# Performance work log

Measured on AMD Instinct MI355X. Metric: run time of the kernel, lower is better.

The kernel has to match this reference:

```python
import jax, jax.numpy as jnp
import numpy as np

D_MODEL = 1024
NUM_HEADS = 16
HEAD_DIM = D_MODEL // NUM_HEADS
ALPHA = 1.0


def setup_inputs() -> dict:
    key = jax.random.key(0)
    ks = jax.random.split(key, 9)
    B, T, D = 2, 2048, D_MODEL
    s = 1.0 / np.sqrt(D)
    inp = {
        "x": jax.random.normal(ks[0], (B, T, D), dtype=jnp.float32),
        "Wq": jax.random.uniform(ks[1], (D, D), jnp.float32, -s, s),
        "bq": jax.random.uniform(ks[2], (D,), jnp.float32, -s, s),
        "Wk": jax.random.uniform(ks[3], (D, D), jnp.float32, -s, s),
        "bk": jax.random.uniform(ks[4], (D,), jnp.float32, -s, s),
        "Wv": jax.random.uniform(ks[5], (D, D), jnp.float32, -s, s),
        "bv": jax.random.uniform(ks[6], (D,), jnp.float32, -s, s),
        "Wo": jax.random.uniform(ks[7], (D, D), jnp.float32, -s, s),
        "bo": jax.random.uniform(ks[8], (D,), jnp.float32, -s, s),
    }
    return inp


def reference(x, Wq, bq, Wk, bk, Wv, bv, Wo, bo):
    B, T, D = x.shape
    H, hd = NUM_HEADS, HEAD_DIM

    def split_heads(y):  # [B,T,D] -> [B,H,T,hd]
        return y.reshape(B, T, H, hd).transpose(0, 2, 1, 3)

    Q = split_heads(x @ Wq.T + bq)
    K = split_heads(x @ Wk.T + bk)
    V = split_heads(x @ Wv.T + bv)

    scores = jnp.einsum('bhid,bhjd->bhij', Q, K) / jnp.sqrt(jnp.float32(hd))

    t = jnp.arange(T)
    delta = t[:, None] - t[None, :]  # [T,T], i - j
    causal_mask = delta < 0          # j > i (strict upper triangle)
    # similarity_power_law decay bias: -(delta)^alpha for delta >= 0, else 0
    decay = jnp.where(causal_mask, 0.0, -(delta.astype(jnp.float32) ** ALPHA))

    scores = jnp.where(causal_mask, -jnp.inf, scores) + decay
    attn = jax.nn.softmax(scores, axis=-1)

    out = jnp.einsum('bhij,bhjd->bhid', attn, V)
    out = out.transpose(0, 2, 1, 3).reshape(B, T, D)
    return out @ Wo.T + bo
```

## Files before the change

### kernel.cpp

```cpp
#include <hip/hip_runtime.h>

#define TT 2048
#define DD 1024
#define HH 16
#define HD 64
#define NTOK 4096

typedef __bf16 bf16x8 __attribute__((ext_vector_type(8)));
typedef short short4v __attribute__((ext_vector_type(4)));
typedef float f32x4 __attribute__((ext_vector_type(4)));
typedef unsigned short ushort8v __attribute__((ext_vector_type(8)));

__device__ __forceinline__ unsigned short f2bf(float f) {
  unsigned u = __float_as_uint(f);
  u += 0x7fffu + ((u >> 16) & 1u);
  return (unsigned short)(u >> 16);
}

#if __has_builtin(__builtin_amdgcn_mfma_f32_16x16x16bf16_1k)
__device__ __forceinline__ f32x4 mfma16(short4v a, short4v b, f32x4 c) {
  return __builtin_amdgcn_mfma_f32_16x16x16bf16_1k(a, b, c, 0, 0, 0);
}
#else
__device__ __forceinline__ f32x4 mfma16(short4v a, short4v b, f32x4 c) {
  asm("v_mfma_f32_16x16x16_bf16 %0, %1, %2, %0\n\ts_nop 7\n\ts_nop 7"
      : "+v"(c) : "v"(a), "v"(b));
  return c;
}
#endif

typedef void __attribute__((address_space(1))) as1_void;
typedef void __attribute__((address_space(3))) as3_void;
__device__ __forceinline__ void gl_lds16(const void* g, void* l) {
  __builtin_amdgcn_global_load_lds((as1_void*)g, (as3_void*)l, 16, 0, 0);
}

__global__ __launch_bounds__(256)
void wcmha_cast_all(const float4* __restrict__ x,  const float4* __restrict__ wq,
                    const float4* __restrict__ wk, const float4* __restrict__ wv,
                    const float4* __restrict__ wo,
                    ushort8v* __restrict__ xb,  ushort8v* __restrict__ wqb,
                    ushort8v* __restrict__ wkb, ushort8v* __restrict__ wvb,
                    ushort8v* __restrict__ wob) {
  const int i = blockIdx.x * 256 + threadIdx.x;
  const float4* src;
  ushort8v* dst;
  int off;
  if (i < 524288) {
    src = x; dst = xb; off = i;
  } else {
    int j = i - 524288;
    int sel = j >> 17;
    off = j & 131071;
    const float4* ws_[4] = {wq, wk, wv, wo};
    ushort8v* wd_[4] = {wqb, wkb, wvb, wob};
    src = ws_[sel]; dst = wd_[sel];
  }
  float4 a = src[off * 2];
  float4 b = src[off * 2 + 1];
  ushort8v o;
  o[0] = f2bf(a.x); o[1] = f2bf(a.y); o[2] = f2bf(a.z); o[3] = f2bf(a.w);
  o[4] = f2bf(b.x); o[5] = f2bf(b.y); o[6] = f2bf(b.z); o[7] = f2bf(b.w);
  dst[off] = o;
}

template <int BN_, bool SWAP>
__device__ __forceinline__ void gemm_db(const unsigned short* __restrict__ X,
                                        const unsigned short* __restrict__ W,
                                        int m0, int n0,
                                        unsigned short* As, unsigned short* Bs,
                                        f32x4 acc[4][BN_ / 32]) {
  constexpr int NI = BN_ / 32;
  constexpr int JB = (BN_ * 4) / 256;
  const int tid = threadIdx.x, wid = tid >> 6, lane = tid & 63;
  const int m = lane & 15, quad = lane >> 4;
  const int wm = (wid >> 1) * 64, wn = (wid & 1) * (BN_ / 2);
  const int xq = (quad ^ ((m >> 1) & 3)) * 8;

  const unsigned short* gA[2];
  const unsigned short* gB[JB];
#pragma unroll
  for (int j = 0; j < 2; ++j) {
    int c = wid * 64 + lane + j * 256;
    gA[j] = X + (size_t)(m0 + (c >> 2)) * DD + ((c & 3) ^ ((c >> 3) & 3)) * 8;
  }
#pragma unroll
  for (int j = 0; j < JB; ++j) {
    int c = wid * 64 + lane + j * 256;
    gB[j] = W + (size_t)(n0 + (c >> 2)) * DD + ((c & 3) ^ ((c >> 3) & 3)) * 8;
  }
  unsigned short* lA[2][2];
  unsigned short* lB[2][JB];
#pragma unroll
  for (int p = 0; p < 2; ++p) {
#pragma unroll
    for (int j = 0; j < 2; ++j)
      lA[p][j] = As + p * (128 * 32) + (wid * 64 + j * 256) * 8;
#pragma unroll
    for (int j = 0; j < JB; ++j)
      lB[p][j] = Bs + p * (BN_ * 32) + (wid * 64 + j * 256) * 8;
  }

#pragma unroll
  for (int i = 0; i < 4; ++i)
#pragma unroll
    for (int j = 0; j < NI; ++j) acc[i][j] = (f32x4){0.f, 0.f, 0.f, 0.f};

#pragma unroll
  for (int j = 0; j < 2; ++j) gl_lds16(gA[j], lA[0][j]);
#pragma unroll
  for (int j = 0; j < JB; ++j) gl_lds16(gB[j], lB[0][j]);

  for (int k = 0; k < 32; ++k) {
    const int p = k & 1;
    __syncthreads();
    if (k < 31) {
      const int k1 = (k + 1) * 32;
#pragma unroll
      for (int j = 0; j < 2; ++j) gl_lds16(gA[j] + k1, lA[p ^ 1][j]);
#pragma unroll
      for (int j = 0; j < JB; ++j) gl_lds16(gB[j] + k1, lB[p ^ 1][j]);
    }
    const unsigned short* ap = As + p * (128 * 32);
    const unsigned short* bp = Bs + p * (BN_ * 32);
    bf16x8 af[4], bf[NI];
#pragma unroll
    for (int mi = 0; mi < 4; ++mi)
      af[mi] = *(const bf16x8*)&ap[(wm + mi * 16 + m) * 32 + xq];
#pragma unroll
    for (int ni = 0; ni < NI; ++ni)
      bf[ni] = *(const bf16x8*)&bp[(wn + ni * 16 + m) * 32 + xq];
#pragma unroll
    for (int mi = 0; mi < 4; ++mi)
#pragma unroll
      for (int ni = 0; ni < NI; ++ni)
        acc[mi][ni] = SWAP
            ? __builtin_amdgcn_mfma_f32_16x16x32_bf16(bf[ni], af[mi], acc[mi][ni], 0, 0, 0)
            : __builtin_amdgcn_mfma_f32_16x16x32_bf16(af[mi], bf[ni], acc[mi][ni], 0, 0, 0);
  }
}

__global__ __launch_bounds__(256)
void wcmha_gemm_qkv(const unsigned short* __restrict__ X,
                    const unsigned short* __restrict__ Wq,
                    const unsigned short* __restrict__ Wk,
                    const unsigned short* __restrict__ Wv,
                    const float* __restrict__ bq, const float* __restrict__ bk,
                    const float* __restrict__ bv,
                    unsigned short* __restrict__ Qb,
                    unsigned short* __restrict__ Kb,
                    unsigned short* __restrict__ Vt) {
  __shared__ unsigned short As[2 * 128 * 32];
  __shared__ unsigned short Bs[2 * 128 * 32];
  const int mat = blockIdx.y >> 3;
  const int m0 = blockIdx.x * 128;
  const int n0 = (blockIdx.y & 7) * 128;

  const int lane = threadIdx.x & 63, wid = threadIdx.x >> 6;
  const int m = lane & 15, quad = lane >> 4;
  const int wm = (wid >> 1) * 64, wn = (wid & 1) * 64;

  f32x4 acc[4][4];
  if (mat < 2) {
    const unsigned short* W = mat ? Wk : Wq;
    const float* bias = mat ? bk : bq;
    unsigned short* dst = mat ? Kb : Qb;
    gemm_db<128, true>(X, W, m0, n0, As, Bs, acc);
#pragma unroll
    for (int mi = 0; mi < 4; ++mi) {
      int row = m0 + wm + mi * 16 + m;
      int b = row >> 11, t = row & (TT - 1);
#pragma unroll
      for (int ni = 0; ni < 4; ++ni) {
        int col0 = n0 + wn + ni * 16 + quad * 4;
        int h = col0 >> 6, d0 = col0 & 63;
        float4 bb = *(const float4*)&bias[col0];
        short4v v;
        v[0] = (short)f2bf(acc[mi][ni][0] + bb.x);
        v[1] = (short)f2bf(acc[mi][ni][1] + bb.y);
        v[2] = (short)f2bf(acc[mi][ni][2] + bb.z);
        v[3] = (short)f2bf(acc[mi][ni][3] + bb.w);
        *(short4v*)&dst[((size_t)(b * HH + h) * TT + t) * HD + d0] = v;
      }
    }
  } else {
    gemm_db<128, false>(X, Wv, m0, n0, As, Bs, acc);
#pragma unroll
    for (int ni = 0; ni < 4; ++ni) {
      int col = n0 + wn + ni * 16 + m;
      int h = col >> 6, d = col & 63;
      float bb = bv[col];
#pragma unroll
      for (int mi = 0; mi < 4; ++mi) {
        int row0 = m0 + wm + mi * 16 + quad * 4;
        int b = row0 >> 11, t0 = row0 & (TT - 1);
        short4v v;
#pragma unroll
        for (int r = 0; r < 4; ++r) v[r] = (short)f2bf(acc[mi][ni][r] + bb);
        *(short4v*)&Vt[((size_t)(b * HH + h) * HD + d) * TT + t0] = v;
      }
    }
  }
}

__global__ __launch_bounds__(256)
void wcmha_gemm_out(const unsigned short* __restrict__ X,
                    const unsigned short* __restrict__ W,
                    const float* __restrict__ bias,
                    float* __restrict__ Y) {
  __shared__ unsigned short As[2 * 128 * 32];
  __shared__ unsigned short Bs[2 * 128 * 32];
  const int m0 = blockIdx.x * 128;
  const int n0 = blockIdx.y * 128;
  const int lane = threadIdx.x & 63, wid = threadIdx.x >> 6;
  const int m = lane & 15, quad = lane >> 4;
  const int wm = (wid >> 1) * 64, wn = (wid & 1) * 64;

  f32x4 acc[4][4];
  gemm_db<128, true>(X, W, m0, n0, As, Bs, acc);

#pragma unroll
  for (int mi = 0; mi < 4; ++mi) {
    int row = m0 + wm + mi * 16 + m;
#pragma unroll
    for (int ni = 0; ni < 4; ++ni) {
      int col0 = n0 + wn + ni * 16 + quad * 4;
      float4 bb = *(const float4*)&bias[col0];
      float4 o;
      o.x = acc[mi][ni][0] + bb.x;
      o.y = acc[mi][ni][1] + bb.y;
      o.z = acc[mi][ni][2] + bb.z;
      o.w = acc[mi][ni][3] + bb.w;
      *(float4*)&Y[(size_t)row * DD + col0] = o;
    }
  }
}

__global__ __launch_bounds__(256)
void wcmha_attn(const unsigned short* __restrict__ Qb,
                const unsigned short* __restrict__ Kb,
                const unsigned short* __restrict__ Vt,
                unsigned short* __restrict__ O) {
  const int wid = threadIdx.x >> 6, lane = threadIdx.x & 63;
  const int gw = (blockIdx.x << 2) + wid;
  const int qt = gw & 127, bh = gw >> 7;
  const int qbase = qt << 4;
  const int il = lane & 15, quad = lane >> 4;
  const int ig = qbase + il;

  const unsigned short* q_ptr = Qb + (size_t)bh * TT * HD;
  const unsigned short* k_ptr = Kb + (size_t)bh * TT * HD;
  const unsigned short* v_ptr = Vt + (size_t)bh * HD * TT;

  const bf16x8 qf0 = *(const bf16x8*)(q_ptr + (size_t)ig * HD + quad * 8);
  const bf16x8 qf1 = *(const bf16x8*)(q_ptr + (size_t)ig * HD + 32 + quad * 8);

  const int j0 = (qbase >= 48) ? qbase - 48 : 0;

  f32x4 st[4];
#pragma unroll
  for (int jt = 0; jt < 4; ++jt) {
    const unsigned short* kp = k_ptr + (size_t)(j0 + jt * 16 + il) * HD;
    bf16x8 k0 = *(const bf16x8*)(kp + quad * 8);
    bf16x8 k1 = *(const bf16x8*)(kp + 32 + quad * 8);
    f32x4 a = {0.f, 0.f, 0.f, 0.f};
    a = __builtin_amdgcn_mfma_f32_16x16x32_bf16(k0, qf0, a, 0, 0, 0);
    a = __builtin_amdgcn_mfma_f32_16x16x32_bf16(k1, qf1, a, 0, 0, 0);
    st[jt] = a;
  }

  float mloc = -3.0e38f;
#pragma unroll
  for (int jt = 0; jt < 4; ++jt)
#pragma unroll
    for (int r = 0; r < 4; ++r) {
      int jg = j0 + jt * 16 + quad * 4 + r;
      float v = (jg > ig) ? -3.0e38f : st[jt][r] * 0.125f - (float)(ig - jg);
      st[jt][r] = v;
      mloc = fmaxf(mloc, v);
    }
  mloc = fmaxf(mloc, __shfl_xor(mloc, 16));
  mloc = fmaxf(mloc, __shfl_xor(mloc, 32));

  float rs = 0.f;
  short4v pf[4];
#pragma unroll
  for (int jt = 0; jt < 4; ++jt)
#pragma unroll
    for (int r = 0; r < 4; ++r) {
      float p = __expf(st[jt][r] - mloc);
      rs += p;
      pf[jt][r] = (short)f2bf(p);
    }
  rs += __shfl_xor(rs, 16);
  rs += __shfl_xor(rs, 32);

  f32x4 o_acc[4];
#pragma unroll
  for (int nt = 0; nt < 4; ++nt) o_acc[nt] = (f32x4){0.f, 0.f, 0.f, 0.f};
#pragma unroll
  for (int jt = 0; jt < 4; ++jt)
#pragma unroll
    for (int nt = 0; nt < 4; ++nt) {
      short4v vf = *(const short4v*)(v_ptr + (size_t)(nt * 16 + il) * TT +
                                     j0 + jt * 16 + quad * 4);
      o_acc[nt] = mfma16(vf, pf[jt], o_acc[nt]);
    }

  const float inv_l = 1.f / rs;
  const int b = bh >> 4, hh = bh & 15;
  unsigned short* ob = O + ((size_t)(b * TT + ig)) * DD + hh * HD;
#pragma unroll
  for (int nt = 0; nt < 4; ++nt) {
    short4v v;
#pragma unroll
    for (int r = 0; r < 4; ++r) v[r] = (short)f2bf(o_acc[nt][r] * inv_l);
    *(short4v*)&ob[nt * 16 + quad * 4] = v;
  }
}

extern "C" void kernel_launch(void* const* d_in, const int* in_sizes, int n_in,
                              void* d_out, int out_size, void* d_ws, size_t ws_size,
                              hipStream_t stream) {
  const float* x  = (const float*)d_in[0];
  const float* Wq = (const float*)d_in[1];
  const float* bq = (const float*)d_in[2];
  const float* Wk = (const float*)d_in[3];
  const float* bk = (const float*)d_in[4];
  const float* Wv = (const float*)d_in[5];
  const float* bv = (const float*)d_in[6];
  const float* Wo = (const float*)d_in[7];
  const float* bo = (const float*)d_in[8];

  char* ws = (char*)d_ws;
  unsigned short* xb  = (unsigned short*)(ws);
  unsigned short* wqb = (unsigned short*)(ws + (8u << 20));
  unsigned short* wkb = wqb + (1u << 20);
  unsigned short* wvb = wkb + (1u << 20);
  unsigned short* wob = wvb + (1u << 20);
  unsigned short* Qb  = (unsigned short*)(ws + (16u << 20));
  unsigned short* Kb  = (unsigned short*)(ws + (24u << 20));
  unsigned short* Vt  = (unsigned short*)(ws + (32u << 20));
  unsigned short* Ob  = xb;

  wcmha_cast_all<<<4096, 256, 0, stream>>>(
      (const float4*)x, (const float4*)Wq, (const float4*)Wk,
      (const float4*)Wv, (const float4*)Wo,
      (ushort8v*)xb, (ushort8v*)wqb, (ushort8v*)wkb, (ushort8v*)wvb,
      (ushort8v*)wob);

  wcmha_gemm_qkv<<<dim3(32, 24), 256, 0, stream>>>(xb, wqb, wkb, wvb,
                                                   bq, bk, bv, Qb, Kb, Vt);

  wcmha_attn<<<1024, 256, 0, stream>>>(Qb, Kb, Vt, Ob);

  wcmha_gemm_out<<<dim3(32, 8), 256, 0, stream>>>(Ob, wob, bo, (float*)d_out);
}
```

Before: 167.2 us.

## Fuse cast, QKV GEMM, attention and output GEMM into one persistent kernel

Replaces the four separate launches with a single persistent kernel of 768 blocks. The stages are separated by a software grid barrier built on an atomic counter, and each stage uses grid-stride or block-index remapping. The goal is to remove per-launch overhead and the drain/fill gaps between kernels. The output GEMM is also retiled to 128x64 tiles over 512 blocks. The change relies on all 768 blocks being co-resident (launch bounds of 3 blocks per CU); if they are not, the barrier deadlocks. The occupancy hint may also constrain registers in the GEMM and attention phases.

```diff
diff --git a/kernel.cpp b/kernel.cpp
--- a/kernel.cpp
+++ b/kernel.cpp
@@ -5,6 +5,7 @@
 #define HH 16
 #define HD 64
 #define NTOK 4096
+#define NBLK 768
 
 typedef __bf16 bf16x8 __attribute__((ext_vector_type(8)));
 typedef short short4v __attribute__((ext_vector_type(4)));
@@ -35,33 +36,21 @@
   __builtin_amdgcn_global_load_lds((as1_void*)g, (as3_void*)l, 16, 0, 0);
 }
 
-__global__ __launch_bounds__(256)
-void wcmha_cast_all(const float4* __restrict__ x,  const float4* __restrict__ wq,
-                    const float4* __restrict__ wk, const float4* __restrict__ wv,
-                    const float4* __restrict__ wo,
-                    ushort8v* __restrict__ xb,  ushort8v* __restrict__ wqb,
-                    ushort8v* __restrict__ wkb, ushort8v* __restrict__ wvb,
-                    ushort8v* __restrict__ wob) {
-  const int i = blockIdx.x * 256 + threadIdx.x;
-  const float4* src;
-  ushort8v* dst;
-  int off;
-  if (i < 524288) {
-    src = x; dst = xb; off = i;
-  } else {
-    int j = i - 524288;
-    int sel = j >> 17;
-    off = j & 131071;
-    const float4* ws_[4] = {wq, wk, wv, wo};
-    ushort8v* wd_[4] = {wqb, wkb, wvb, wob};
-    src = ws_[sel]; dst = wd_[sel];
-  }
-  float4 a = src[off * 2];
-  float4 b = src[off * 2 + 1];
-  ushort8v o;
-  o[0] = f2bf(a.x); o[1] = f2bf(a.y); o[2] = f2bf(a.z); o[3] = f2bf(a.w);
-  o[4] = f2bf(b.x); o[5] = f2bf(b.y); o[6] = f2bf(b.z); o[7] = f2bf(b.w);
-  dst[off] = o;
+__device__ unsigned g_bar = 0;
+
+__device__ __forceinline__ void grid_sync() {
+  __syncthreads();
+  if (threadIdx.x == 0) {
+    __builtin_amdgcn_fence(__ATOMIC_RELEASE, "agent");
+    unsigned old = __hip_atomic_fetch_add(&g_bar, 1u, __ATOMIC_RELAXED,
+                                          __HIP_MEMORY_SCOPE_AGENT);
+    unsigned target = (old / NBLK + 1u) * NBLK;
+    while (__hip_atomic_load(&g_bar, __ATOMIC_RELAXED,
+                             __HIP_MEMORY_SCOPE_AGENT) < target)
+      __builtin_amdgcn_s_sleep(1);
+    __builtin_amdgcn_fence(__ATOMIC_ACQUIRE, "agent");
+  }
+  __syncthreads();
 }
 
 template <int BN_, bool SWAP>
@@ -140,182 +129,208 @@
   }
 }
 
-__global__ __launch_bounds__(256)
-void wcmha_gemm_qkv(const unsigned short* __restrict__ X,
-                    const unsigned short* __restrict__ Wq,
-                    const unsigned short* __restrict__ Wk,
-                    const unsigned short* __restrict__ Wv,
-                    const float* __restrict__ bq, const float* __restrict__ bk,
-                    const float* __restrict__ bv,
-                    unsigned short* __restrict__ Qb,
-                    unsigned short* __restrict__ Kb,
-                    unsigned short* __restrict__ Vt) {
+__global__ __launch_bounds__(256, 3)
+void wcmha_fused(const float4* __restrict__ xf,  const float4* __restrict__ wqf,
+                 const float4* __restrict__ wkf, const float4* __restrict__ wvf,
+                 const float4* __restrict__ wof,
+                 const float* __restrict__ bq, const float* __restrict__ bk,
+                 const float* __restrict__ bv, const float* __restrict__ bo,
+                 unsigned short* __restrict__ xb,  unsigned short* __restrict__ wqb,
+                 unsigned short* __restrict__ wkb, unsigned short* __restrict__ wvb,
+                 unsigned short* __restrict__ wob,
+                 unsigned short* __restrict__ Qb, unsigned short* __restrict__ Kb,
+                 unsigned short* __restrict__ Vt, float* __restrict__ Y) {
   __shared__ unsigned short As[2 * 128 * 32];
   __shared__ unsigned short Bs[2 * 128 * 32];
-  const int mat = blockIdx.y >> 3;
-  const int m0 = blockIdx.x * 128;
-  const int n0 = (blockIdx.y & 7) * 128;
-
-  const int lane = threadIdx.x & 63, wid = threadIdx.x >> 6;
+
+  const int tid = threadIdx.x;
+  const int lane = tid & 63, wid = tid >> 6;
   const int m = lane & 15, quad = lane >> 4;
-  const int wm = (wid >> 1) * 64, wn = (wid & 1) * 64;
-
-  f32x4 acc[4][4];
-  if (mat < 2) {
-    const unsigned short* W = mat ? Wk : Wq;
-    const float* bias = mat ? bk : bq;
-    unsigned short* dst = mat ? Kb : Qb;
-    gemm_db<128, true>(X, W, m0, n0, As, Bs, acc);
+
+  for (int i = (int)blockIdx.x * 256 + tid; i < 1048576; i += NBLK * 256) {
+    const float4* src;
+    ushort8v* dst;
+    int off;
+    if (i < 524288) {
+      src = xf; dst = (ushort8v*)xb; off = i;
+    } else {
+      int j = i - 524288;
+      int sel = j >> 17;
+      off = j & 131071;
+      const float4* ws_[4] = {wqf, wkf, wvf, wof};
+      ushort8v* wd_[4] = {(ushort8v*)wqb, (ushort8v*)wkb, (ushort8v*)wvb,
+                          (ushort8v*)wob};
+      src = ws_[sel]; dst = wd_[sel];
+    }
+    float4 a = src[off * 2];
+    float4 b = src[off * 2 + 1];
+    ushort8v o;
+    o[0] = f2bf(a.x); o[1] = f2bf(a.y); o[2] = f2bf(a.z); o[3] = f2bf(a.w);
+    o[4] = f2bf(b.x); o[5] = f2bf(b.y); o[6] = f2bf(b.z); o[7] = f2bf(b.w);
+    dst[off] = o;
+  }
+
+  grid_sync();
+
+  {
+    const int bx = (int)blockIdx.x & 31;
+    const int by = (int)blockIdx.x >> 5;
+    const int mat = by >> 3;
+    const int m0 = bx * 128;
+    const int n0 = (by & 7) * 128;
+    const int wm = (wid >> 1) * 64, wn = (wid & 1) * 64;
+
+    f32x4 acc[4][4];
+    if (mat < 2) {
+      const unsigned short* W = mat ? wkb : wqb;
+      const float* bias = mat ? bk : bq;
+      unsigned short* dst = mat ? Kb : Qb;
+      gemm_db<128, true>(xb, W, m0, n0, As, Bs, acc);
+#pragma unroll
+      for (int mi = 0; mi < 4; ++mi) {
+        int row = m0 + wm + mi * 16 + m;
+        int b = row >> 11, t = row & (TT - 1);
+#pragma unroll
+        for (int ni = 0; ni < 4; ++ni) {
+          int col0 = n0 + wn + ni * 16 + quad * 4;
+          int h = col0 >> 6, d0 = col0 & 63;
+          float4 bb = *(const float4*)&bias[col0];
+          short4v v;
+          v[0] = (short)f2bf(acc[mi][ni][0] + bb.x);
+          v[1] = (short)f2bf(acc[mi][ni][1] + bb.y);
+          v[2] = (short)f2bf(acc[mi][ni][2] + bb.z);
+          v[3] = (short)f2bf(acc[mi][ni][3] + bb.w);
+          *(short4v*)&dst[((size_t)(b * HH + h) * TT + t) * HD + d0] = v;
+        }
+      }
+    } else {
+      gemm_db<128, false>(xb, wvb, m0, n0, As, Bs, acc);
+#pragma unroll
+      for (int ni = 0; ni < 4; ++ni) {
+        int col = n0 + wn + ni * 16 + m;
+        int h = col >> 6, d = col & 63;
+        float bb = bv[col];
+#pragma unroll
+        for (int mi = 0; mi < 4; ++mi) {
+          int row0 = m0 + wm + mi * 16 + quad * 4;
+          int b = row0 >> 11, t0 = row0 & (TT - 1);
+          short4v v;
+#pragma unroll
+          for (int r = 0; r < 4; ++r) v[r] = (short)f2bf(acc[mi][ni][r] + bb);
+          *(short4v*)&Vt[((size_t)(b * HH + h) * HD + d) * TT + t0] = v;
+        }
+      }
+    }
+  }
+
+  grid_sync();
+
+  {
+    unsigned short* O = xb;
+    const int il = m;
+    for (int gw = ((int)blockIdx.x << 2) + wid; gw < 4096; gw += NBLK * 4) {
+      const int qt = gw & 127, bh = gw >> 7;
+      const int qbase = qt << 4;
+      const int ig = qbase + il;
+
+      const unsigned short* q_ptr = Qb + (size_t)bh * TT * HD;
+      const unsigned short* k_ptr = Kb + (size_t)bh * TT * HD;
+      const unsigned short* v_ptr = Vt + (size_t)bh * HD * TT;
+
+      const bf16x8 qf0 = *(const bf16x8*)(q_ptr + (size_t)ig * HD + quad * 8);
+      const bf16x8 qf1 = *(const bf16x8*)(q_ptr + (size_t)ig * HD + 32 + quad * 8);
+
+      const int j0 = (qbase >= 48) ? qbase - 48 : 0;
+
+      f32x4 st[4];
+#pragma unroll
+      for (int jt = 0; jt < 4; ++jt) {
+        const unsigned short* kp = k_ptr + (size_t)(j0 + jt * 16 + il) * HD;
+        bf16x8 k0 = *(const bf16x8*)(kp + quad * 8);
+        bf16x8 k1 = *(const bf16x8*)(kp + 32 + quad * 8);
+        f32x4 a = {0.f, 0.f, 0.f, 0.f};
+        a = __builtin_amdgcn_mfma_f32_16x16x32_bf16(k0, qf0, a, 0, 0, 0);
+        a = __builtin_amdgcn_mfma_f32_16x16x32_bf16(k1, qf1, a, 0, 0, 0);
+        st[jt] = a;
+      }
+
+      float mloc = -3.0e38f;
+#pragma unroll
+      for (int jt = 0; jt < 4; ++jt)
+#pragma unroll
+        for (int r = 0; r < 4; ++r) {
+          int jg = j0 + jt * 16 + quad * 4 + r;
+          float v = (jg > ig) ? -3.0e38f : st[jt][r] * 0.125f - (float)(ig - jg);
+          st[jt][r] = v;
+          mloc = fmaxf(mloc, v);
+        }
+      mloc = fmaxf(mloc, __shfl_xor(mloc, 16));
+      mloc = fmaxf(mloc, __shfl_xor(mloc, 32));
+
+      float rs = 0.f;
+      short4v pf[4];
+#pragma unroll
+      for (int jt = 0; jt < 4; ++jt)
+#pragma unroll
+        for (int r = 0; r < 4; ++r) {
+          float p = __expf(st[jt][r] - mloc);
+          rs += p;
+          pf[jt][r] = (short)f2bf(p);
+        }
+      rs += __shfl_xor(rs, 16);
+      rs += __shfl_xor(rs, 32);
+
+      f32x4 o_acc[4];
+#pragma unroll
+      for (int nt = 0; nt < 4; ++nt) o_acc[nt] = (f32x4){0.f, 0.f, 0.f, 0.f};
+#pragma unroll
+      for (int jt = 0; jt < 4; ++jt)
+#pragma unroll
+        for (int nt = 0; nt < 4; ++nt) {
+          short4v vf = *(const short4v*)(v_ptr + (size_t)(nt * 16 + il) * TT +
+                                         j0 + jt * 16 + quad * 4);
+          o_acc[nt] = mfma16(vf, pf[jt], o_acc[nt]);
+        }
+
+      const float inv_l = 1.f / rs;
+      const int b = bh >> 4, hh = bh & 15;
+      unsigned short* ob = O + ((size_t)(b * TT + ig)) * DD + hh * HD;
+#pragma unroll
+      for (int nt = 0; nt < 4; ++nt) {
+        short4v v;
+#pragma unroll
+        for (int r = 0; r < 4; ++r) v[r] = (short)f2bf(o_acc[nt][r] * inv_l);
+        *(short4v*)&ob[nt * 16 + quad * 4] = v;
+      }
+    }
+  }
+
+  grid_sync();
+
+  if (blockIdx.x < 512) {
+    const unsigned short* Ob = xb;
+    const int m0 = ((int)blockIdx.x & 31) * 128;
+    const int n0 = ((int)blockIdx.x >> 5) * 64;
+    const int wm = (wid >> 1) * 64, wn = (wid & 1) * 32;
+
+    f32x4 acc[4][2];
+    gemm_db<64, true>(Ob, wob, m0, n0, As, Bs, acc);
+
 #pragma unroll
     for (int mi = 0; mi < 4; ++mi) {
       int row = m0 + wm + mi * 16 + m;
-      int b = row >> 11, t = row & (TT - 1);
-#pragma unroll
-      for (int ni = 0; ni < 4; ++ni) {
+#pragma unroll
+      for (int ni = 0; ni < 2; ++ni) {
         int col0 = n0 + wn + ni * 16 + quad * 4;
-        int h = col0 >> 6, d0 = col0 & 63;
-        float4 bb = *(const float4*)&bias[col0];
-        short4v v;
-        v[0] = (short)f2bf(acc[mi][ni][0] + bb.x);
-        v[1] = (short)f2bf(acc[mi][ni][1] + bb.y);
-        v[2] = (short)f2bf(acc[mi][ni][2] + bb.z);
-        v[3] = (short)f2bf(acc[mi][ni][3] + bb.w);
-        *(short4v*)&dst[((size_t)(b * HH + h) * TT + t) * HD + d0] = v;
-      }
-    }
-  } else {
-    gemm_db<128, false>(X, Wv, m0, n0, As, Bs, acc);
-#pragma unroll
-    for (int ni = 0; ni < 4; ++ni) {
-      int col = n0 + wn + ni * 16 + m;
-      int h = col >> 6, d = col & 63;
-      float bb = bv[col];
-#pragma unroll
-      for (int mi = 0; mi < 4; ++mi) {
-        int row0 = m0 + wm + mi * 16 + quad * 4;
-        int b = row0 >> 11, t0 = row0 & (TT - 1);
-        short4v v;
-#pragma unroll
-        for (int r = 0; r < 4; ++r) v[r] = (short)f2bf(acc[mi][ni][r] + bb);
-        *(short4v*)&Vt[((size_t)(b * HH + h) * HD + d) * TT + t0] = v;
-      }
-    }
-  }
-}
-
-__global__ __launch_bounds__(256)
-void wcmha_gemm_out(const unsigned short* __restrict__ X,
-                    const unsigned short* __restrict__ W,
-                    const float* __restrict__ bias,
-                    float* __restrict__ Y) {
-  __shared__ unsigned short As[2 * 128 * 32];
-  __shared__ unsigned short Bs[2 * 128 * 32];
-  const int m0 = blockIdx.x * 128;
-  const int n0 = blockIdx.y * 128;
-  const int lane = threadIdx.x & 63, wid = threadIdx.x >> 6;
-  const int m = lane & 15, quad = lane >> 4;
-  const int wm = (wid >> 1) * 64, wn = (wid & 1) * 64;
-
-  f32x4 acc[4][4];
-  gemm_db<128, true>(X, W, m0, n0, As, Bs, acc);
-
-#pragma unroll
-  for (int mi = 0; mi < 4; ++mi) {
-    int row = m0 + wm + mi * 16 + m;
-#pragma unroll
-    for (int ni = 0; ni < 4; ++ni) {
-      int col0 = n0 + wn + ni * 16 + quad * 4;
-      float4 bb = *(const float4*)&bias[col0];
-      float4 o;
-      o.x = acc[mi][ni][0] + bb.x;
-      o.y = acc[mi][ni][1] + bb.y;
-      o.z = acc[mi][ni][2] + bb.z;
-      o.w = acc[mi][ni][3] + bb.w;
-      *(float4*)&Y[(size_t)row * DD + col0] = o;
-    }
-  }
-}
-
-__global__ __launch_bounds__(256)
-void wcmha_attn(const unsigned short* __restrict__ Qb,
-                const unsigned short* __restrict__ Kb,
-                const unsigned short* __restrict__ Vt,
-                unsigned short* __restrict__ O) {
-  const int wid = threadIdx.x >> 6, lane = threadIdx.x & 63;
-  const int gw = (blockIdx.x << 2) + wid;
-  const int qt = gw & 127, bh = gw >> 7;
-  const int qbase = qt << 4;
-  const int il = lane & 15, quad = lane >> 4;
-  const int ig = qbase + il;
-
-  const unsigned short* q_ptr = Qb + (size_t)bh * TT * HD;
-  const unsigned short* k_ptr = Kb + (size_t)bh * TT * HD;
-  const unsigned short* v_ptr = Vt + (size_t)bh * HD * TT;
-
-  const bf16x8 qf0 = *(const bf16x8*)(q_ptr + (size_t)ig * HD + quad * 8);
-  const bf16x8 qf1 = *(const bf16x8*)(q_ptr + (size_t)ig * HD + 32 + quad * 8);
-
-  const int j0 = (qbase >= 48) ? qbase - 48 : 0;
-
-  f32x4 st[4];
-#pragma unroll
-  for (int jt = 0; jt < 4; ++jt) {
-    const unsigned short* kp = k_ptr + (size_t)(j0 + jt * 16 + il) * HD;
-    bf16x8 k0 = *(const bf16x8*)(kp + quad * 8);
-    bf16x8 k1 = *(const bf16x8*)(kp + 32 + quad * 8);
-    f32x4 a = {0.f, 0.f, 0.f, 0.f};
-    a = __builtin_amdgcn_mfma_f32_16x16x32_bf16(k0, qf0, a, 0, 0, 0);
-    a = __builtin_amdgcn_mfma_f32_16x16x32_bf16(k1, qf1, a, 0, 0, 0);
-    st[jt] = a;
-  }
-
-  float mloc = -3.0e38f;
-#pragma unroll
-  for (int jt = 0; jt < 4; ++jt)
-#pragma unroll
-    for (int r = 0; r < 4; ++r) {
-      int jg = j0 + jt * 16 + quad * 4 + r;
-      float v = (jg > ig) ? -3.0e38f : st[jt][r] * 0.125f - (float)(ig - jg);
-      st[jt][r] = v;
-      mloc = fmaxf(mloc, v);
-    }
-  mloc = fmaxf(mloc, __shfl_xor(mloc, 16));
-  mloc = fmaxf(mloc, __shfl_xor(mloc, 32));
-
-  float rs = 0.f;
-  short4v pf[4];
-#pragma unroll
-  for (int jt = 0; jt < 4; ++jt)
-#pragma unroll
-    for (int r = 0; r < 4; ++r) {
-      float p = __expf(st[jt][r] - mloc);
-      rs += p;
-      pf[jt][r] = (short)f2bf(p);
-    }
-  rs += __shfl_xor(rs, 16);
-  rs += __shfl_xor(rs, 32);
-
-  f32x4 o_acc[4];
-#pragma unroll
-  for (int nt = 0; nt < 4; ++nt) o_acc[nt] = (f32x4){0.f, 0.f, 0.f, 0.f};
-#pragma unroll
-  for (int jt = 0; jt < 4; ++jt)
-#pragma unroll
-    for (int nt = 0; nt < 4; ++nt) {
-      short4v vf = *(const short4v*)(v_ptr + (size_t)(nt * 16 + il) * TT +
-                                     j0 + jt * 16 + quad * 4);
-      o_acc[nt] = mfma16(vf, pf[jt], o_acc[nt]);
-    }
-
-  const float inv_l = 1.f / rs;
-  const int b = bh >> 4, hh = bh & 15;
-  unsigned short* ob = O + ((size_t)(b * TT + ig)) * DD + hh * HD;
-#pragma unroll
-  for (int nt = 0; nt < 4; ++nt) {
-    short4v v;
-#pragma unroll
-    for (int r = 0; r < 4; ++r) v[r] = (short)f2bf(o_acc[nt][r] * inv_l);
-    *(short4v*)&ob[nt * 16 + quad * 4] = v;
+        float4 bb = *(const float4*)&bo[col0];
+        float4 o;
+        o.x = acc[mi][ni][0] + bb.x;
+        o.y = acc[mi][ni][1] + bb.y;
+        o.z = acc[mi][ni][2] + bb.z;
+        o.w = acc[mi][ni][3] + bb.w;
+        *(float4*)&Y[(size_t)row * DD + col0] = o;
+      }
+    }
   }
 }
 
@@ -341,18 +356,10 @@
   unsigned short* Qb  = (unsigned short*)(ws + (16u << 20));
   unsigned short* Kb  = (unsigned short*)(ws + (24u << 20));
   unsigned short* Vt  = (unsigned short*)(ws + (32u << 20));
-  unsigned short* Ob  = xb;
-
-  wcmha_cast_all<<<4096, 256, 0, stream>>>(
+
+  wcmha_fused<<<NBLK, 256, 0, stream>>>(
       (const float4*)x, (const float4*)Wq, (const float4*)Wk,
       (const float4*)Wv, (const float4*)Wo,
-      (ushort8v*)xb, (ushort8v*)wqb, (ushort8v*)wkb, (ushort8v*)wvb,
-      (ushort8v*)wob);
-
-  wcmha_gemm_qkv<<<dim3(32, 24), 256, 0, stream>>>(xb, wqb, wkb, wvb,
-                                                   bq, bk, bv, Qb, Kb, Vt);
-
-  wcmha_attn<<<1024, 256, 0, stream>>>(Qb, Kb, Vt, Ob);
-
-  wcmha_gemm_out<<<dim3(32, 8), 256, 0, stream>>>(Ob, wob, bo, (float*)d_out);
-}
+      bq, bk, bv, bo,
+      xb, wqb, wkb, wvb, wob, Qb, Kb, Vt, (float*)d_out);
+}
```

Measured after the change: 353.1 us. +111.2%, slower.

## Replace QKV GEMM with 256x256 ping-pong pipelined kernel; shrink out-proj tiles

Applied to the files above, without the earlier changes.

The QKV projection now runs as a 512-thread kernel with 256x256 tiles. It uses an explicit four-phase software pipeline: async global-to-LDS loads are interleaved with MFMA bursts, and s_waitcnt, barriers and setprio are placed by hand. This should cut per-tile global traffic and hide load latency better. The V output now uses the same accumulator layout as Q and K, writing the transposed Vt as scalar stores, which may coalesce poorly. The output-projection GEMM switches to 128x64 tiles to launch twice as many blocks, filling more CUs.

```diff
diff --git a/kernel.cpp b/kernel.cpp
--- a/kernel.cpp
+++ b/kernel.cpp
@@ -4,7 +4,6 @@
 #define DD 1024
 #define HH 16
 #define HD 64
-#define NTOK 4096
 
 typedef __bf16 bf16x8 __attribute__((ext_vector_type(8)));
 typedef short short4v __attribute__((ext_vector_type(4)));
@@ -140,39 +139,161 @@
   }
 }
 
-__global__ __launch_bounds__(256)
-void wcmha_gemm_qkv(const unsigned short* __restrict__ X,
-                    const unsigned short* __restrict__ Wq,
-                    const unsigned short* __restrict__ Wk,
-                    const unsigned short* __restrict__ Wv,
-                    const float* __restrict__ bq, const float* __restrict__ bk,
-                    const float* __restrict__ bv,
-                    unsigned short* __restrict__ Qb,
-                    unsigned short* __restrict__ Kb,
-                    unsigned short* __restrict__ Vt) {
-  __shared__ unsigned short As[2 * 128 * 32];
-  __shared__ unsigned short Bs[2 * 128 * 32];
-  const int mat = blockIdx.y >> 3;
-  const int m0 = blockIdx.x * 128;
-  const int n0 = (blockIdx.y & 7) * 128;
-
-  const int lane = threadIdx.x & 63, wid = threadIdx.x >> 6;
+__global__ __launch_bounds__(512, 2)
+void wcmha_qkv8(const unsigned short* __restrict__ X,
+                const unsigned short* __restrict__ Wq,
+                const unsigned short* __restrict__ Wk,
+                const unsigned short* __restrict__ Wv,
+                const float* __restrict__ bq, const float* __restrict__ bk,
+                const float* __restrict__ bv,
+                unsigned short* __restrict__ Qb,
+                unsigned short* __restrict__ Kb,
+                unsigned short* __restrict__ Vt) {
+  __shared__ unsigned short As[2 * 2 * 256 * 32];
+  __shared__ unsigned short Bs[2 * 2 * 256 * 32];
+  const int tid = threadIdx.x;
+  const int lane = tid & 63, wid = tid >> 6;
   const int m = lane & 15, quad = lane >> 4;
-  const int wm = (wid >> 1) * 64, wn = (wid & 1) * 64;
-
-  f32x4 acc[4][4];
+  const int wr = wid >> 2, wc = wid & 3;
+
+  const int mt = blockIdx.x & 15, nt = blockIdx.x >> 4;
+  const int m0 = mt * 256;
+  const int mat = nt >> 2;
+  const int n0w = (nt & 3) * 256;
+  const unsigned short* W = (mat == 0) ? Wq : ((mat == 1) ? Wk : Wv);
+
+  const int srow = tid >> 2;
+  const int schunk = ((tid & 3) ^ ((tid >> 3) & 3)) * 8;
+  const unsigned short* gA[2];
+  const unsigned short* gB[2];
+  gA[0] = X + (size_t)(m0 + srow) * DD + schunk;
+  gA[1] = X + (size_t)(m0 + 128 + srow) * DD + schunk;
+  gB[0] = W + (size_t)(n0w + srow) * DD + schunk;
+  gB[1] = W + (size_t)(n0w + 128 + srow) * DD + schunk;
+  const int ldst = tid * 8;
+
+#define STAGE_A(buf, ks, koff)                                            \
+  {                                                                       \
+    gl_lds16(gA[0] + (koff), &As[((buf) * 2 + (ks)) * 8192 + ldst]);      \
+    gl_lds16(gA[1] + (koff), &As[((buf) * 2 + (ks)) * 8192 + 4096 + ldst]); \
+  }
+#define STAGE_B(buf, ks, koff)                                            \
+  {                                                                       \
+    gl_lds16(gB[0] + (koff), &Bs[((buf) * 2 + (ks)) * 8192 + ldst]);      \
+    gl_lds16(gB[1] + (koff), &Bs[((buf) * 2 + (ks)) * 8192 + 4096 + ldst]); \
+  }
+
+  f32x4 acc[8][4];
+#pragma unroll
+  for (int i = 0; i < 8; ++i)
+#pragma unroll
+    for (int j = 0; j < 4; ++j) acc[i][j] = (f32x4){0.f, 0.f, 0.f, 0.f};
+
+  STAGE_A(0, 0, 0) STAGE_B(0, 0, 0)
+  STAGE_A(0, 1, 32) STAGE_B(0, 1, 32)
+  STAGE_A(1, 0, 64) STAGE_B(1, 0, 64)
+
+  const int xq = (quad ^ ((m >> 1) & 3)) * 8;
+  const int arow = wr * 128 + m;
+  const int brow = wc * 64 + m;
+
+#pragma unroll 1
+  for (int kt = 0; kt < 16; ++kt) {
+    const int cur = kt & 1, nxt = cur ^ 1;
+    const unsigned short* a0 = &As[(cur * 2 + 0) * 8192];
+    const unsigned short* b0 = &Bs[(cur * 2 + 0) * 8192];
+    const unsigned short* a1 = &As[(cur * 2 + 1) * 8192];
+    const unsigned short* b1 = &Bs[(cur * 2 + 1) * 8192];
+    const int kA = (kt + 1) * 64, kB2 = (kt + 2) * 64;
+    bf16x8 af[4], bf[4];
+
+    if (kt < 15) { asm volatile("s_waitcnt vmcnt(8)" ::: "memory"); }
+    else         { asm volatile("s_waitcnt vmcnt(4)" ::: "memory"); }
+    __builtin_amdgcn_s_barrier();
+    __builtin_amdgcn_sched_barrier(0);
+#pragma unroll
+    for (int mi = 0; mi < 4; ++mi)
+      af[mi] = *(const bf16x8*)&a0[(arow + mi * 16) * 32 + xq];
+#pragma unroll
+    for (int ni = 0; ni < 4; ++ni)
+      bf[ni] = *(const bf16x8*)&b0[(brow + ni * 16) * 32 + xq];
+    if (kt < 15) STAGE_A(nxt, 1, kA + 32)
+    asm volatile("s_waitcnt lgkmcnt(0)" ::: "memory");
+    __builtin_amdgcn_sched_barrier(0);
+    __builtin_amdgcn_s_setprio(1);
+#pragma unroll
+    for (int mi = 0; mi < 4; ++mi)
+#pragma unroll
+      for (int ni = 0; ni < 4; ++ni)
+        acc[mi][ni] = __builtin_amdgcn_mfma_f32_16x16x32_bf16(bf[ni], af[mi], acc[mi][ni], 0, 0, 0);
+    __builtin_amdgcn_s_setprio(0);
+
+    __builtin_amdgcn_s_barrier();
+    __builtin_amdgcn_sched_barrier(0);
+#pragma unroll
+    for (int mi = 0; mi < 4; ++mi)
+      af[mi] = *(const bf16x8*)&a0[(arow + (mi + 4) * 16) * 32 + xq];
+    if (kt < 15) STAGE_B(nxt, 1, kA + 32)
+    asm volatile("s_waitcnt lgkmcnt(0)" ::: "memory");
+    __builtin_amdgcn_sched_barrier(0);
+    __builtin_amdgcn_s_setprio(1);
+#pragma unroll
+    for (int mi = 0; mi < 4; ++mi)
+#pragma unroll
+      for (int ni = 0; ni < 4; ++ni)
+        acc[mi + 4][ni] = __builtin_amdgcn_mfma_f32_16x16x32_bf16(bf[ni], af[mi], acc[mi + 4][ni], 0, 0, 0);
+    __builtin_amdgcn_s_setprio(0);
+
+    if (kt < 15) { asm volatile("s_waitcnt vmcnt(8)" ::: "memory"); }
+    else         { asm volatile("s_waitcnt vmcnt(0)" ::: "memory"); }
+    __builtin_amdgcn_s_barrier();
+    __builtin_amdgcn_sched_barrier(0);
+#pragma unroll
+    for (int mi = 0; mi < 4; ++mi)
+      af[mi] = *(const bf16x8*)&a1[(arow + mi * 16) * 32 + xq];
+#pragma unroll
+    for (int ni = 0; ni < 4; ++ni)
+      bf[ni] = *(const bf16x8*)&b1[(brow + ni * 16) * 32 + xq];
+    if (kt < 14) STAGE_A(cur, 0, kB2)
+    asm volatile("s_waitcnt lgkmcnt(0)" ::: "memory");
+    __builtin_amdgcn_sched_barrier(0);
+    __builtin_amdgcn_s_setprio(1);
+#pragma unroll
+    for (int mi = 0; mi < 4; ++mi)
+#pragma unroll
+      for (int ni = 0; ni < 4; ++ni)
+        acc[mi][ni] = __builtin_amdgcn_mfma_f32_16x16x32_bf16(bf[ni], af[mi], acc[mi][ni], 0, 0, 0);
+    __builtin_amdgcn_s_setprio(0);
+
+    __builtin_amdgcn_s_barrier();
+    __builtin_amdgcn_sched_barrier(0);
+#pragma unroll
+    for (int mi = 0; mi < 4; ++mi)
+      af[mi] = *(const bf16x8*)&a1[(arow + (mi + 4) * 16) * 32 + xq];
+    if (kt < 14) STAGE_B(cur, 0, kB2)
+    asm volatile("s_waitcnt lgkmcnt(0)" ::: "memory");
+    __builtin_amdgcn_sched_barrier(0);
+    __builtin_amdgcn_s_setprio(1);
+#pragma unroll
+    for (int mi = 0; mi < 4; ++mi)
+#pragma unroll
+      for (int ni = 0; ni < 4; ++ni)
+        acc[mi + 4][ni] = __builtin_amdgcn_mfma_f32_16x16x32_bf16(bf[ni], af[mi], acc[mi + 4][ni], 0, 0, 0);
+    __builtin_amdgcn_s_setprio(0);
+  }
+#undef STAGE_A
+#undef STAGE_B
+
   if (mat < 2) {
-    const unsigned short* W = mat ? Wk : Wq;
     const float* bias = mat ? bk : bq;
     unsigned short* dst = mat ? Kb : Qb;
-    gemm_db<128, true>(X, W, m0, n0, As, Bs, acc);
-#pragma unroll
-    for (int mi = 0; mi < 4; ++mi) {
-      int row = m0 + wm + mi * 16 + m;
+#pragma unroll
+    for (int mi = 0; mi < 8; ++mi) {
+      int row = m0 + wr * 128 + mi * 16 + m;
       int b = row >> 11, t = row & (TT - 1);
 #pragma unroll
       for (int ni = 0; ni < 4; ++ni) {
-        int col0 = n0 + wn + ni * 16 + quad * 4;
+        int col0 = n0w + wc * 64 + ni * 16 + quad * 4;
         int h = col0 >> 6, d0 = col0 & 63;
         float4 bb = *(const float4*)&bias[col0];
         short4v v;
@@ -184,20 +305,20 @@
       }
     }
   } else {
-    gemm_db<128, false>(X, Wv, m0, n0, As, Bs, acc);
-#pragma unroll
-    for (int ni = 0; ni < 4; ++ni) {
-      int col = n0 + wn + ni * 16 + m;
-      int h = col >> 6, d = col & 63;
-      float bb = bv[col];
-#pragma unroll
-      for (int mi = 0; mi < 4; ++mi) {
-        int row0 = m0 + wm + mi * 16 + quad * 4;
-        int b = row0 >> 11, t0 = row0 & (TT - 1);
-        short4v v;
-#pragma unroll
-        for (int r = 0; r < 4; ++r) v[r] = (short)f2bf(acc[mi][ni][r] + bb);
-        *(short4v*)&Vt[((size_t)(b * HH + h) * HD + d) * TT + t0] = v;
+#pragma unroll
+    for (int mi = 0; mi < 8; ++mi) {
+      int row = m0 + wr * 128 + mi * 16 + m;
+      int b = row >> 11, t = row & (TT - 1);
+#pragma unroll
+      for (int ni = 0; ni < 4; ++ni) {
+        int col0 = n0w + wc * 64 + ni * 16 + quad * 4;
+        int h = col0 >> 6, d0 = col0 & 63;
+#pragma unroll
+        for (int r = 0; r < 4; ++r) {
+          float bb = bv[col0 + r];
+          Vt[((size_t)(b * HH + h) * HD + d0 + r) * TT + t] =
+              f2bf(acc[mi][ni][r] + bb);
+        }
       }
     }
   }
@@ -209,21 +330,21 @@
                     const float* __restrict__ bias,
                     float* __restrict__ Y) {
   __shared__ unsigned short As[2 * 128 * 32];
-  __shared__ unsigned short Bs[2 * 128 * 32];
+  __shared__ unsigned short Bs[2 * 64 * 32];
   const int m0 = blockIdx.x * 128;
-  const int n0 = blockIdx.y * 128;
+  const int n0 = blockIdx.y * 64;
   const int lane = threadIdx.x & 63, wid = threadIdx.x >> 6;
   const int m = lane & 15, quad = lane >> 4;
-  const int wm = (wid >> 1) * 64, wn = (wid & 1) * 64;
-
-  f32x4 acc[4][4];
-  gemm_db<128, true>(X, W, m0, n0, As, Bs, acc);
+  const int wm = (wid >> 1) * 64, wn = (wid & 1) * 32;
+
+  f32x4 acc[4][2];
+  gemm_db<64, true>(X, W, m0, n0, As, Bs, acc);
 
 #pragma unroll
   for (int mi = 0; mi < 4; ++mi) {
     int row = m0 + wm + mi * 16 + m;
 #pragma unroll
-    for (int ni = 0; ni < 4; ++ni) {
+    for (int ni = 0; ni < 2; ++ni) {
       int col0 = n0 + wn + ni * 16 + quad * 4;
       float4 bb = *(const float4*)&bias[col0];
       float4 o;
@@ -349,10 +470,10 @@
       (ushort8v*)xb, (ushort8v*)wqb, (ushort8v*)wkb, (ushort8v*)wvb,
       (ushort8v*)wob);
 
-  wcmha_gemm_qkv<<<dim3(32, 24), 256, 0, stream>>>(xb, wqb, wkb, wvb,
-                                                   bq, bk, bv, Qb, Kb, Vt);
+  wcmha_qkv8<<<192, 512, 0, stream>>>(xb, wqb, wkb, wvb,
+                                      bq, bk, bv, Qb, Kb, Vt);
 
   wcmha_attn<<<1024, 256, 0, stream>>>(Qb, Kb, Vt, Ob);
 
-  wcmha_gemm_out<<<dim3(32, 8), 256, 0, stream>>>(Ob, wob, bo, (float*)d_out);
-}
+  wcmha_gemm_out<<<dim3(32, 16), 256, 0, stream>>>(Ob, wob, bo, (float*)d_out);
+}
```

Result: faster. 163.8 us (-2.0%).
